# Kernel optimization log

Measured on AMD Instinct MI355X. Metric: run time of the kernel, lower is better.

The kernel has to match this reference:

```python
import jax, jax.numpy as jnp
import numpy as np

NUM_IDS = 8
K_HALF = 5            # k = K//2
DIM = 2048
CP_DIM = DIM // 8     # cp_ratio = 8
N = NUM_IDS * 2 * K_HALF
H, W = 24, 8


def _kaiming(key, out_c, in_c):
    # kaiming_normal_(fan_out, relu) for a 1x1 conv: std = sqrt(2/out_c)
    return jax.random.normal(key, (out_c, in_c), dtype=jnp.float32) * np.sqrt(2.0 / out_c)


def setup_inputs() -> dict:
    key = jax.random.key(0)
    ks = jax.random.split(key, 8)
    inputs = jax.random.normal(ks[0], (N, DIM, H, W), dtype=jnp.float32)
    # PK batch: each identity has K_HALF samples with sub==1 and K_HALF with sub==0
    labels = jnp.repeat(jnp.arange(NUM_IDS, dtype=jnp.int64), 2 * K_HALF)
    sub = jnp.tile(jnp.concatenate([jnp.ones(K_HALF, jnp.int64), jnp.zeros(K_HALF, jnp.int64)]), NUM_IDS)
    return {
        "inputs": inputs,
        "labels": labels,
        "sub": sub,
        "W_ri": _kaiming(ks[1], CP_DIM, DIM),
        "W_rv": _kaiming(ks[2], CP_DIM, DIM),
        "W_ci": _kaiming(ks[3], DIM, K_HALF * CP_DIM),
        "W_cv": _kaiming(ks[4], DIM, K_HALF * CP_DIM),
        "W_f": _kaiming(ks[5], DIM, 2 * DIM),
    }


def reference(inputs, labels, sub, W_ri, W_rv, W_ci, W_cv, W_f):
    n, c, h, w = inputs.shape
    cp = W_ri.shape[0]
    k = W_ci.shape[1] // cp
    n_half = n // 2
    x = jax.lax.stop_gradient(inputs)  # .detach() in the original

    def branch(sub_mask_val, Wr, Wc):
        # indices of samples in this sub-group (order-preserving, like boolean mask)
        sidx = jnp.nonzero(sub == sub_mask_val, size=n_half)[0]
        xs = jnp.einsum('nchw,oc->nohw', x[sidx], Wr)       # [n_half, cp, h, w]
        lab = labels[sidx]                                   # [n_half]
        # for each batch sample, the k positions in the sub-group with matching label
        match = labels[:, None] == lab[None, :]              # [n, n_half]
        pos = jnp.where(match, jnp.arange(n_half)[None, :], n_half)
        gidx = jnp.sort(pos, axis=1)[:, :k]                  # [n, k]
        aff = xs[gidx].reshape(n, k * cp, h, w)              # gather + channel-stack
        return jax.nn.relu(jnp.einsum('nchw,oc->nohw', aff, Wc))

    s_i = branch(1, W_ri, W_ci)   # sub == 1
    s_v = branch(0, W_rv, W_cv)   # sub == 0
    x_fuse = jax.nn.sigmoid(
        jnp.einsum('nchw,oc->nohw', jnp.concatenate([s_i, s_v], axis=1), W_f))
    return inputs + inputs * x_fuse
```

## Files before the change

### kernel.cpp

```cpp
#include <hip/hip_runtime.h>

typedef unsigned short u16;
typedef unsigned int u32;
typedef __bf16 bf16_t;
typedef bf16_t bf16x8 __attribute__((ext_vector_type(8)));
typedef float f32x4 __attribute__((ext_vector_type(4)));

#define DIM 2048
#define HW  192
#define CP  256
#define NB  80

__device__ __forceinline__ u16 f2b(float f) {
    u32 u = __float_as_uint(f);
    u32 r = (u + 0x7FFFu + ((u >> 16) & 1u)) >> 16;
    return (u16)r;
}

__device__ __forceinline__ void g2l16(const void* g, void* l) {
    __builtin_amdgcn_global_load_lds(
        (const __attribute__((address_space(1))) u32*)g,
        (__attribute__((address_space(3))) u32*)l, 16, 0, 0);
}

template<int ACT, bool OUTF32, typename F>
__device__ __forceinline__ void gemm_core(F actAddr, int arstride,
    const u16* __restrict__ Wp, int wstride, int K,
    void* __restrict__ outp, int M)
{
    __shared__ u16 act_s[96 * 32];
    __shared__ u16 w_s[128 * 32];
    const int t    = threadIdx.x;
    const int w    = t >> 6;
    const int lane = t & 63;
    const int ln   = lane & 15;
    const int q    = lane >> 4;
    const int qe   = q ^ ((ln >> 1) & 3);

    f32x4 acc[6][4];
    #pragma unroll
    for (int i = 0; i < 6; ++i)
        #pragma unroll
        for (int j = 0; j < 4; ++j) acc[i][j] = (f32x4){0.f, 0.f, 0.f, 0.f};

    int a_off[6], b_off[4];
    #pragma unroll
    for (int i = 0; i < 6; ++i) a_off[i] = (i * 16 + ln) * 32 + qe * 8;
    #pragma unroll
    for (int j = 0; j < 4; ++j) b_off[j] = (w * 64 + j * 16 + ln) * 32 + qe * 8;

    for (int k0 = 0; k0 < K; k0 += 32) {
        const u16* ap = actAddr(k0);
        __syncthreads();
        #pragma unroll
        for (int r = 0; r < 4; ++r) {
            int idx = r * 128 + t;
            int row = idx >> 2, pc = idx & 3;
            int lc  = pc ^ ((row >> 1) & 3);
            g2l16(Wp + (size_t)row * wstride + k0 + lc * 8, (void*)(w_s + idx * 8));
        }
        #pragma unroll
        for (int r = 0; r < 3; ++r) {
            int idx = r * 128 + t;
            int row = idx >> 2, pc = idx & 3;
            int lc  = pc ^ ((row >> 1) & 3);
            g2l16(ap + (size_t)row * arstride + lc * 8, (void*)(act_s + idx * 8));
        }
        __syncthreads();
        bf16x8 af[6], bf[4];
        #pragma unroll
        for (int i = 0; i < 6; ++i) af[i] = *(const bf16x8*)(act_s + a_off[i]);
        #pragma unroll
        for (int j = 0; j < 4; ++j) bf[j] = *(const bf16x8*)(w_s + b_off[j]);
        #pragma unroll
        for (int i = 0; i < 6; ++i)
            #pragma unroll
            for (int j = 0; j < 4; ++j)
                acc[i][j] = __builtin_amdgcn_mfma_f32_16x16x32_bf16(
                    af[i], bf[j], acc[i][j], 0, 0, 0);
    }
    #pragma unroll
    for (int i = 0; i < 6; ++i) {
        #pragma unroll
        for (int j = 0; j < 4; ++j) {
            #pragma unroll
            for (int r = 0; r < 4; ++r) {
                float v = acc[i][j][r];
                if (ACT == 1) v = v > 0.f ? v : 0.f;
                int nl = i * 16 + q * 4 + r;
                int ml = w * 64 + j * 16 + ln;
                if (OUTF32) ((float*)outp)[(size_t)nl * M + ml] = v;
                else        ((u16*)outp)[(size_t)nl * M + ml] = f2b(v);
            }
        }
    }
}

__global__ __launch_bounds__(128) void proj_g(const u16* __restrict__ xt,
    const int* __restrict__ sub, int nbase,
    const u16* __restrict__ Wri, const u16* __restrict__ Wrv,
    u16* __restrict__ projt)
{
    const int z = blockIdx.z, bn = blockIdx.x, bm = blockIdx.y;
    const int n = nbase + z;
    const u16* act = xt + (size_t)z * (HW * DIM) + (size_t)bn * 96 * DIM;
    const u16* Wp  = ((sub[n] != 0) ? Wri : Wrv) + (size_t)bm * 128 * DIM;
    u16* outp = projt + (size_t)n * (HW * CP) + (size_t)(bn * 96) * CP + bm * 128;
    auto f = [=](int k0) { return act + k0; };
    gemm_core<0, false>(f, DIM, Wp, DIM, DIM, outp, CP);
}

__global__ __launch_bounds__(128) void compose_g(const u16* __restrict__ projt,
    const u16* __restrict__ Wci, const u16* __restrict__ Wcv,
    u16* __restrict__ st)
{
    const int z = blockIdx.z, br = z >> 3, id = z & 7;
    const int bn = blockIdx.x, bm = blockIdx.y;
    const u16* base = projt + (size_t)(id * 10 + br * 5) * (HW * CP) + (size_t)bn * 96 * CP;
    const u16* Wp   = (br ? Wcv : Wci) + (size_t)bm * 128 * 1280;
    u16* outp = st + (size_t)(id * 2 + br) * (HW * DIM) + (size_t)bn * 96 * DIM + bm * 128;
    auto f = [=](int k0) { return base + (size_t)(k0 >> 8) * (HW * CP) + (k0 & 255); };
    gemm_core<1, false>(f, CP, Wp, 1280, 1280, outp, DIM);
}

__global__ __launch_bounds__(128) void fuse_g(const u16* __restrict__ st,
    const u16* __restrict__ Wf, float* __restrict__ fuset2)
{
    const int z = blockIdx.z, h = z >> 3, id = z & 7;
    const int bn = blockIdx.x, bm = blockIdx.y;
    const u16* base = st + (size_t)(id * 2 + h) * (HW * DIM) + (size_t)bn * 96 * DIM;
    const u16* Wp   = Wf + (size_t)bm * 128 * (2 * DIM) + (size_t)h * DIM;
    float* outp = fuset2 + (size_t)h * (8 * HW * DIM) + (size_t)id * (HW * DIM)
                + (size_t)bn * 96 * DIM + bm * 128;
    auto f = [=](int k0) { return base + k0; };
    gemm_core<0, true>(f, DIM, Wp, 2 * DIM, DIM, outp, DIM);
}

__global__ __launch_bounds__(256) void xt_k(const float* __restrict__ x,
                                            u16* __restrict__ xt)
{
    __shared__ float ts[64][65];
    const int z = blockIdx.z;
    const int p0 = blockIdx.x * 64, c0 = blockIdx.y * 64;
    const int t = threadIdx.x, l = t & 63;
    #pragma unroll
    for (int i = 0; i < 16; ++i) {
        int cl = (t >> 6) * 16 + i;
        ts[cl][l] = x[((size_t)z * DIM + c0 + cl) * HW + p0 + l];
    }
    __syncthreads();
    #pragma unroll
    for (int i = 0; i < 16; ++i) {
        int pl = (t >> 6) * 16 + i;
        xt[((size_t)z * HW + p0 + pl) * DIM + c0 + l] = f2b(ts[l][pl]);
    }
}

__global__ __launch_bounds__(256) void fuse_tr(const float* __restrict__ fuset2,
                                               float* __restrict__ fuse)
{
    __shared__ float ts[64][65];
    const int id = blockIdx.z;
    const int c0 = blockIdx.x * 64, p0 = blockIdx.y * 64;
    const int t = threadIdx.x, l = t & 63;
    const float* f0 = fuset2;
    const float* f1 = fuset2 + (size_t)8 * HW * DIM;
    #pragma unroll
    for (int i = 0; i < 16; ++i) {
        int pl = (t >> 6) * 16 + i;
        size_t a = ((size_t)id * HW + p0 + pl) * DIM + c0 + l;
        float v = f0[a] + f1[a];
        ts[pl][l] = 1.f / (1.f + __expf(-v));
    }
    __syncthreads();
    #pragma unroll
    for (int i = 0; i < 16; ++i) {
        int cl = (t >> 6) * 16 + i;
        fuse[((size_t)id * DIM + c0 + cl) * HW + p0 + l] = ts[l][cl];
    }
}

__global__ __launch_bounds__(256) void wcvt(
    const float* __restrict__ a0, const float* __restrict__ a1,
    const float* __restrict__ a2, const float* __restrict__ a3,
    const float* __restrict__ a4,
    u16* __restrict__ o0, u16* __restrict__ o1, u16* __restrict__ o2,
    u16* __restrict__ o3, u16* __restrict__ o4)
{
    size_t off = ((size_t)blockIdx.x * 256 + threadIdx.x) * 4;
    const float* s; u16* d;
    if (off < 524288)            { s = a0; d = o0; }
    else if ((off -= 524288) < 524288)   { s = a1; d = o1; }
    else if ((off -= 524288) < 2621440)  { s = a2; d = o2; }
    else if ((off -= 2621440) < 2621440) { s = a3; d = o3; }
    else                         { off -= 2621440; s = a4; d = o4; }
    float4 v = *(const float4*)(s + off);
    ushort4 p;
    p.x = f2b(v.x); p.y = f2b(v.y); p.z = f2b(v.z); p.w = f2b(v.w);
    *(ushort4*)(d + off) = p;
}

__global__ __launch_bounds__(256) void final_kernel(const float* __restrict__ x,
    const int* __restrict__ labels, const float* __restrict__ fusebuf,
    float* __restrict__ out)
{
    const size_t e = ((size_t)blockIdx.x * blockDim.x + threadIdx.x) * 4;
    const int n   = (int)(e / ((size_t)DIM * HW));
    const int rem = (int)(e % ((size_t)DIM * HW));
    const int id  = labels[n];
    float4 xv = *reinterpret_cast<const float4*>(x + e);
    float4 fv = *reinterpret_cast<const float4*>(fusebuf + (size_t)id * DIM * HW + rem);
    float4 o;
    o.x = xv.x + xv.x * fv.x;
    o.y = xv.y + xv.y * fv.y;
    o.z = xv.z + xv.z * fv.z;
    o.w = xv.w + xv.w * fv.w;
    *reinterpret_cast<float4*>(out + e) = o;
}

extern "C" void kernel_launch(void* const* d_in, const int* in_sizes, int n_in,
                              void* d_out, int out_size, void* d_ws, size_t ws_size,
                              hipStream_t stream) {
    const float* x      = (const float*)d_in[0];
    const int*   labels = (const int*)d_in[1];
    const int*   sub    = (const int*)d_in[2];
    const float* Wri    = (const float*)d_in[3];
    const float* Wrv    = (const float*)d_in[4];
    const float* Wci    = (const float*)d_in[5];
    const float* Wcv    = (const float*)d_in[6];
    const float* Wf     = (const float*)d_in[7];
    float* out = (float*)d_out;
    char* ws = (char*)d_ws;

    const bool full = ws_size >= (size_t)112721920;
    const size_t R1 = full ? (size_t)62914560 : (size_t)25165824;

    u16*   xtbuf  = (u16*)ws;
    float* fuset2 = (float*)ws;
    char*  wreg   = ws + R1;
    u16* Wri_b = (u16*)(wreg);
    u16* Wrv_b = (u16*)(wreg + 1048576);
    u16* Wci_b = (u16*)(wreg + 2097152);
    u16* Wcv_b = (u16*)(wreg + 7340032);
    u16* Wf_b  = (u16*)(wreg + 12582912);
    float* fuse = (float*)(wreg + 12582912);
    u16* projt = (u16*)(wreg + 29360128);
    u16* stb   = (u16*)(wreg + 29360128 + 7864320);

    wcvt<<<14336, 256, 0, stream>>>(Wri, Wrv, Wci, Wcv, Wf,
                                    Wri_b, Wrv_b, Wci_b, Wcv_b, Wf_b);
    const int nchunk = full ? 1 : 4;
    const int cs = NB / nchunk;
    for (int c = 0; c < nchunk; ++c) {
        xt_k  <<<dim3(3, 32, cs), 256, 0, stream>>>(x + (size_t)c * cs * DIM * HW, xtbuf);
        proj_g<<<dim3(2, 2, cs), 128, 0, stream>>>(xtbuf, sub, c * cs, Wri_b, Wrv_b, projt);
    }
    compose_g<<<dim3(2, 16, 16), 128, 0, stream>>>(projt, Wci_b, Wcv_b, stb);
    fuse_g   <<<dim3(2, 16, 16), 128, 0, stream>>>(stb, Wf_b, fuset2);
    fuse_tr  <<<dim3(32, 3, 8), 256, 0, stream>>>(fuset2, fuse);
    final_kernel<<<30720, 256, 0, stream>>>(x, labels, fuse, out);
}
```

Measured before the change: 451.6 us.

## Double-buffer GEMM LDS, switch to 32x32 MFMA, split fuse K, vectorize transpose

The shared GEMM core now double-buffers its LDS tiles so the next K-slice loads while the current one computes, and uses 32x32x16 bf16 MFMA with fewer, larger accumulators. The fuse GEMM is split into four K-partitions to double its grid, and the transpose kernel sums four fp32 partial buffers. The input transpose uses float4 loads and ushort4 stores, and the final kernel uses 32-bit index math. The workspace layout is rearranged and needs more memory, and the extra partial buffers add fp32 traffic.

```diff
diff --git a/kernel.cpp b/kernel.cpp
--- a/kernel.cpp
+++ b/kernel.cpp
@@ -4,7 +4,7 @@
 typedef unsigned int u32;
 typedef __bf16 bf16_t;
 typedef bf16_t bf16x8 __attribute__((ext_vector_type(8)));
-typedef float f32x4 __attribute__((ext_vector_type(4)));
+typedef float f32x16 __attribute__((ext_vector_type(16)));
 
 #define DIM 2048
 #define HW  192
@@ -28,67 +28,80 @@
     const u16* __restrict__ Wp, int wstride, int K,
     void* __restrict__ outp, int M)
 {
-    __shared__ u16 act_s[96 * 32];
-    __shared__ u16 w_s[128 * 32];
+    __shared__ u16 act_s[2][96 * 32];
+    __shared__ u16 w_s[2][128 * 32];
     const int t    = threadIdx.x;
     const int w    = t >> 6;
     const int lane = t & 63;
-    const int ln   = lane & 15;
-    const int q    = lane >> 4;
-    const int qe   = q ^ ((ln >> 1) & 3);
-
-    f32x4 acc[6][4];
-    #pragma unroll
-    for (int i = 0; i < 6; ++i)
-        #pragma unroll
-        for (int j = 0; j < 4; ++j) acc[i][j] = (f32x4){0.f, 0.f, 0.f, 0.f};
-
-    int a_off[6], b_off[4];
-    #pragma unroll
-    for (int i = 0; i < 6; ++i) a_off[i] = (i * 16 + ln) * 32 + qe * 8;
-    #pragma unroll
-    for (int j = 0; j < 4; ++j) b_off[j] = (w * 64 + j * 16 + ln) * 32 + qe * 8;
-
-    for (int k0 = 0; k0 < K; k0 += 32) {
+    const int ln   = lane & 31;
+    const int q2   = lane >> 5;
+    const int swz  = (ln >> 1) & 3;
+
+    f32x16 acc[3][2];
+    #pragma unroll
+    for (int i = 0; i < 3; ++i)
+        #pragma unroll
+        for (int j = 0; j < 2; ++j)
+            #pragma unroll
+            for (int r = 0; r < 16; ++r) acc[i][j][r] = 0.f;
+
+    auto stage = [&](int buf, int k0) {
         const u16* ap = actAddr(k0);
-        __syncthreads();
         #pragma unroll
         for (int r = 0; r < 4; ++r) {
             int idx = r * 128 + t;
             int row = idx >> 2, pc = idx & 3;
             int lc  = pc ^ ((row >> 1) & 3);
-            g2l16(Wp + (size_t)row * wstride + k0 + lc * 8, (void*)(w_s + idx * 8));
+            g2l16(Wp + (size_t)row * wstride + k0 + lc * 8, (void*)(w_s[buf] + idx * 8));
         }
         #pragma unroll
         for (int r = 0; r < 3; ++r) {
             int idx = r * 128 + t;
             int row = idx >> 2, pc = idx & 3;
             int lc  = pc ^ ((row >> 1) & 3);
-            g2l16(ap + (size_t)row * arstride + lc * 8, (void*)(act_s + idx * 8));
-        }
+            g2l16(ap + (size_t)row * arstride + lc * 8, (void*)(act_s[buf] + idx * 8));
+        }
+    };
+
+    auto compute = [&](int buf) {
+        #pragma unroll
+        for (int s = 0; s < 2; ++s) {
+            bf16x8 af[3], bf[2];
+            const int phys = (s * 2 + q2) ^ swz;
+            #pragma unroll
+            for (int i = 0; i < 3; ++i)
+                af[i] = *(const bf16x8*)(act_s[buf] + (i * 32 + ln) * 32 + phys * 8);
+            #pragma unroll
+            for (int j = 0; j < 2; ++j)
+                bf[j] = *(const bf16x8*)(w_s[buf] + (w * 64 + j * 32 + ln) * 32 + phys * 8);
+            #pragma unroll
+            for (int i = 0; i < 3; ++i)
+                #pragma unroll
+                for (int j = 0; j < 2; ++j)
+                    acc[i][j] = __builtin_amdgcn_mfma_f32_32x32x16_bf16(
+                        af[i], bf[j], acc[i][j], 0, 0, 0);
+        }
+    };
+
+    stage(0, 0);
+    const int iters = K / 32;
+    for (int it = 0; it < iters; ++it) {
+        int b = it & 1;
         __syncthreads();
-        bf16x8 af[6], bf[4];
-        #pragma unroll
-        for (int i = 0; i < 6; ++i) af[i] = *(const bf16x8*)(act_s + a_off[i]);
-        #pragma unroll
-        for (int j = 0; j < 4; ++j) bf[j] = *(const bf16x8*)(w_s + b_off[j]);
-        #pragma unroll
-        for (int i = 0; i < 6; ++i)
-            #pragma unroll
-            for (int j = 0; j < 4; ++j)
-                acc[i][j] = __builtin_amdgcn_mfma_f32_16x16x32_bf16(
-                    af[i], bf[j], acc[i][j], 0, 0, 0);
-    }
-    #pragma unroll
-    for (int i = 0; i < 6; ++i) {
-        #pragma unroll
-        for (int j = 0; j < 4; ++j) {
-            #pragma unroll
-            for (int r = 0; r < 4; ++r) {
+        if (it + 1 < iters) stage(b ^ 1, (it + 1) * 32);
+        compute(b);
+    }
+
+    #pragma unroll
+    for (int i = 0; i < 3; ++i) {
+        #pragma unroll
+        for (int j = 0; j < 2; ++j) {
+            #pragma unroll
+            for (int r = 0; r < 16; ++r) {
                 float v = acc[i][j][r];
                 if (ACT == 1) v = v > 0.f ? v : 0.f;
-                int nl = i * 16 + q * 4 + r;
-                int ml = w * 64 + j * 16 + ln;
+                int nl = i * 32 + (r & 3) + 8 * (r >> 2) + 4 * q2;
+                int ml = w * 64 + j * 32 + ln;
                 if (OUTF32) ((float*)outp)[(size_t)nl * M + ml] = v;
                 else        ((u16*)outp)[(size_t)nl * M + ml] = f2b(v);
             }
@@ -124,16 +137,17 @@
 }
 
 __global__ __launch_bounds__(128) void fuse_g(const u16* __restrict__ st,
-    const u16* __restrict__ Wf, float* __restrict__ fuset2)
+    const u16* __restrict__ Wf, float* __restrict__ fuset4)
 {
     const int z = blockIdx.z, h = z >> 3, id = z & 7;
     const int bn = blockIdx.x, bm = blockIdx.y;
-    const u16* base = st + (size_t)(id * 2 + h) * (HW * DIM) + (size_t)bn * 96 * DIM;
-    const u16* Wp   = Wf + (size_t)bm * 128 * (2 * DIM) + (size_t)h * DIM;
-    float* outp = fuset2 + (size_t)h * (8 * HW * DIM) + (size_t)id * (HW * DIM)
+    const u16* base = st + (size_t)(id * 2 + (h >> 1)) * (HW * DIM)
+                    + (size_t)bn * 96 * DIM + (h & 1) * 1024;
+    const u16* Wp   = Wf + (size_t)bm * 128 * (2 * DIM) + (size_t)h * 1024;
+    float* outp = fuset4 + (size_t)h * (8 * HW * DIM) + (size_t)id * (HW * DIM)
                 + (size_t)bn * 96 * DIM + bm * 128;
     auto f = [=](int k0) { return base + k0; };
-    gemm_core<0, true>(f, DIM, Wp, 2 * DIM, DIM, outp, DIM);
+    gemm_core<0, true>(f, DIM, Wp, 2 * DIM, 1024, outp, DIM);
 }
 
 __global__ __launch_bounds__(256) void xt_k(const float* __restrict__ x,
@@ -142,34 +156,40 @@
     __shared__ float ts[64][65];
     const int z = blockIdx.z;
     const int p0 = blockIdx.x * 64, c0 = blockIdx.y * 64;
-    const int t = threadIdx.x, l = t & 63;
-    #pragma unroll
-    for (int i = 0; i < 16; ++i) {
-        int cl = (t >> 6) * 16 + i;
-        ts[cl][l] = x[((size_t)z * DIM + c0 + cl) * HW + p0 + l];
+    const int t = threadIdx.x;
+    #pragma unroll
+    for (int r = 0; r < 4; ++r) {
+        int idx = r * 256 + t;
+        int c = idx >> 4, p4 = (idx & 15) * 4;
+        float4 v = *(const float4*)(x + ((size_t)z * DIM + c0 + c) * HW + p0 + p4);
+        ts[c][p4 + 0] = v.x; ts[c][p4 + 1] = v.y;
+        ts[c][p4 + 2] = v.z; ts[c][p4 + 3] = v.w;
     }
     __syncthreads();
     #pragma unroll
-    for (int i = 0; i < 16; ++i) {
-        int pl = (t >> 6) * 16 + i;
-        xt[((size_t)z * HW + p0 + pl) * DIM + c0 + l] = f2b(ts[l][pl]);
-    }
-}
-
-__global__ __launch_bounds__(256) void fuse_tr(const float* __restrict__ fuset2,
+    for (int r = 0; r < 4; ++r) {
+        int idx = r * 256 + t;
+        int p = idx >> 4, c4 = (idx & 15) * 4;
+        ushort4 o;
+        o.x = f2b(ts[c4 + 0][p]); o.y = f2b(ts[c4 + 1][p]);
+        o.z = f2b(ts[c4 + 2][p]); o.w = f2b(ts[c4 + 3][p]);
+        *(ushort4*)(xt + ((size_t)z * HW + p0 + p) * DIM + c0 + c4) = o;
+    }
+}
+
+__global__ __launch_bounds__(256) void fuse_tr(const float* __restrict__ fuset4,
                                                float* __restrict__ fuse)
 {
     __shared__ float ts[64][65];
     const int id = blockIdx.z;
     const int c0 = blockIdx.x * 64, p0 = blockIdx.y * 64;
     const int t = threadIdx.x, l = t & 63;
-    const float* f0 = fuset2;
-    const float* f1 = fuset2 + (size_t)8 * HW * DIM;
+    const size_t hs = (size_t)8 * HW * DIM;
     #pragma unroll
     for (int i = 0; i < 16; ++i) {
         int pl = (t >> 6) * 16 + i;
         size_t a = ((size_t)id * HW + p0 + pl) * DIM + c0 + l;
-        float v = f0[a] + f1[a];
+        float v = fuset4[a] + fuset4[a + hs] + fuset4[a + 2 * hs] + fuset4[a + 3 * hs];
         ts[pl][l] = 1.f / (1.f + __expf(-v));
     }
     __syncthreads();
@@ -189,11 +209,11 @@
 {
     size_t off = ((size_t)blockIdx.x * 256 + threadIdx.x) * 4;
     const float* s; u16* d;
-    if (off < 524288)            { s = a0; d = o0; }
+    if (off < 524288)                    { s = a0; d = o0; }
     else if ((off -= 524288) < 524288)   { s = a1; d = o1; }
     else if ((off -= 524288) < 2621440)  { s = a2; d = o2; }
     else if ((off -= 2621440) < 2621440) { s = a3; d = o3; }
-    else                         { off -= 2621440; s = a4; d = o4; }
+    else                                 { off -= 2621440; s = a4; d = o4; }
     float4 v = *(const float4*)(s + off);
     ushort4 p;
     p.x = f2b(v.x); p.y = f2b(v.y); p.z = f2b(v.z); p.w = f2b(v.w);
@@ -204,9 +224,9 @@
     const int* __restrict__ labels, const float* __restrict__ fusebuf,
     float* __restrict__ out)
 {
-    const size_t e = ((size_t)blockIdx.x * blockDim.x + threadIdx.x) * 4;
-    const int n   = (int)(e / ((size_t)DIM * HW));
-    const int rem = (int)(e % ((size_t)DIM * HW));
+    const u32 e = ((u32)blockIdx.x * 256u + threadIdx.x) * 4u;
+    const u32 n   = e / ((u32)DIM * HW);
+    const u32 rem = e % ((u32)DIM * HW);
     const int id  = labels[n];
     float4 xv = *reinterpret_cast<const float4*>(x + e);
     float4 fv = *reinterpret_cast<const float4*>(fusebuf + (size_t)id * DIM * HW + rem);
@@ -232,20 +252,19 @@
     float* out = (float*)d_out;
     char* ws = (char*)d_ws;
 
-    const bool full = ws_size >= (size_t)112721920;
-    const size_t R1 = full ? (size_t)62914560 : (size_t)25165824;
-
-    u16*   xtbuf  = (u16*)ws;
-    float* fuset2 = (float*)ws;
-    char*  wreg   = ws + R1;
-    u16* Wri_b = (u16*)(wreg);
-    u16* Wrv_b = (u16*)(wreg + 1048576);
-    u16* Wci_b = (u16*)(wreg + 2097152);
-    u16* Wcv_b = (u16*)(wreg + 7340032);
-    u16* Wf_b  = (u16*)(wreg + 12582912);
-    float* fuse = (float*)(wreg + 12582912);
-    u16* projt = (u16*)(wreg + 29360128);
-    u16* stb   = (u16*)(wreg + 29360128 + 7864320);
+    const bool full = ws_size >= (size_t)175636480;
+    const size_t xtb = full ? (size_t)62914560 : (size_t)15728640;
+
+    u16* Wri_b = (u16*)(ws);
+    u16* Wrv_b = (u16*)(ws + 1048576);
+    u16* Wci_b = (u16*)(ws + 2097152);
+    u16* Wcv_b = (u16*)(ws + 7340032);
+    u16* Wf_b  = (u16*)(ws + 12582912);
+    u16* xtbuf = (u16*)(ws + 29360128);
+    u16* projt = (u16*)(ws + 29360128 + xtb);
+    u16* stb   = (u16*)(ws + 29360128 + xtb + 7864320);
+    float* fuset4 = (float*)(ws + 29360128 + xtb + 7864320 + 12582912);
+    float* fuse   = (float*)(ws + 29360128 + xtb + 7864320 + 12582912 + 50331648);
 
     wcvt<<<14336, 256, 0, stream>>>(Wri, Wrv, Wci, Wcv, Wf,
                                     Wri_b, Wrv_b, Wci_b, Wcv_b, Wf_b);
@@ -256,7 +275,7 @@
         proj_g<<<dim3(2, 2, cs), 128, 0, stream>>>(xtbuf, sub, c * cs, Wri_b, Wrv_b, projt);
     }
     compose_g<<<dim3(2, 16, 16), 128, 0, stream>>>(projt, Wci_b, Wcv_b, stb);
-    fuse_g   <<<dim3(2, 16, 16), 128, 0, stream>>>(stb, Wf_b, fuset2);
-    fuse_tr  <<<dim3(32, 3, 8), 256, 0, stream>>>(fuset2, fuse);
+    fuse_g   <<<dim3(2, 16, 32), 128, 0, stream>>>(stb, Wf_b, fuset4);
+    fuse_tr  <<<dim3(32, 3, 8), 256, 0, stream>>>(fuset4, fuse);
     final_kernel<<<30720, 256, 0, stream>>>(x, labels, fuse, out);
 }
```

New measurement: 445.2 us. No clear change (-1.4%).
